# Kernel optimization log

Hardware: AMD Instinct MI355X
Metric: run time of the kernel (lower is better)

The kernel has to match this reference:

```python
import jax, jax.numpy as jnp
import numpy as np

NH, NW = 5, 5          # attn_neighborhood_size (odd -> symmetric 'same' padding)
HEADS, HEAD_DIM = 8, 64
DIM = 512              # == heads*head_dim, but project_out=True since heads>1
B, HMAP, WMAP = 4, 64, 64
N = HMAP * WMAP


def local_expand(t, height, width):
    """Equivalent of impulse-filter conv2d neighbor gather.

    t: [b, heads, n, d] -> [b, heads, n, NH*NW, d]
    neighbor f=(i,j) of pixel (p,q) is t[p+i-NH//2, q+j-NW//2], zero-padded.
    """
    b, h, n, d = t.shape
    y = t.reshape(b, h, height, width, d)
    ph, pw = NH // 2, NW // 2
    yp = jnp.pad(y, ((0, 0), (0, 0), (ph, ph), (pw, pw), (0, 0)))
    # fixed small loop over the 25 window offsets (row-major = filter order)
    slabs = [yp[:, :, i:i + height, j:j + width, :]
             for i in range(NH) for j in range(NW)]
    out = jnp.stack(slabs, axis=4)  # [b, h, H, W, F, d]
    return out.reshape(b, h, n, NH * NW, d)


def setup_inputs() -> dict:
    key = jax.random.key(0)
    k1, k2, k3, k4 = jax.random.split(key, 4)
    inner = HEADS * HEAD_DIM
    x = jax.random.normal(k1, (B, N, DIM), dtype=jnp.float32)
    # torch Linear weights are [out_features, in_features]
    w_qkv = jax.random.normal(k2, (3 * inner, DIM), dtype=jnp.float32) * (DIM ** -0.5)
    w_out = jax.random.normal(k3, (DIM, inner), dtype=jnp.float32) * (inner ** -0.5)
    b_out = jax.random.normal(k4, (DIM,), dtype=jnp.float32) * 0.01
    return {"x": x, "w_qkv": w_qkv, "w_out": w_out, "b_out": b_out,
            "h": HMAP, "w": WMAP}


def reference(x, w_qkv, w_out, b_out, h, w):
    b, n, _ = x.shape
    scale = HEAD_DIM ** -0.5
    qkv = x @ w_qkv.T                                   # [b, n, 3*inner]
    q, k, v = jnp.split(qkv, 3, axis=-1)
    def to_heads(t):
        return t.reshape(b, n, HEADS, HEAD_DIM).transpose(0, 2, 1, 3)  # b h n d
    q, k, v = to_heads(q), to_heads(k), to_heads(v)
    k_loc = local_expand(k, h, w)                       # [b, h, n, F, d]
    v_loc = local_expand(v, h, w)
    dots = jnp.einsum('bhnd,bhnfd->bhnf', q, k_loc) * scale
    attn = jax.nn.softmax(dots, axis=-1)
    out = jnp.einsum('bhnf,bhnfd->bhnd', attn, v_loc)   # [b, h, n, d]
    out = out.transpose(0, 2, 1, 3).reshape(b, n, HEADS * HEAD_DIM)
    return out @ w_out.T + b_out                        # dropout=0 (eval)
```

## Files before the change

### kernel.cpp

```cpp
#include <hip/hip_runtime.h>
#include <cstddef>
#include <cstdint>


namespace {

typedef short s16x8 __attribute__((ext_vector_type(8)));
typedef unsigned short u16x8 __attribute__((ext_vector_type(8)));
typedef float f32x4 __attribute__((ext_vector_type(4)));

constexpr int kHeads = 8;
constexpr int kN = 4096;
constexpr float kScale = 0.125f;

__device__ inline float b2f(unsigned short u) {
  return __uint_as_float((unsigned)u << 16);
}
__device__ inline float blo(unsigned u) {
  return __uint_as_float(u << 16);
}
__device__ inline float bhi(unsigned u) {
  return __uint_as_float(u & 0xffff0000u);
}
__device__ inline unsigned short f2b(float x) {
  unsigned u = __float_as_uint(x);
  return (unsigned short)((u + 0x7fffu + ((u >> 16) & 1u)) >> 16);
}

__device__ __forceinline__ float dot2bf(float d, unsigned a, unsigned b) {
  asm("v_dot2_f32_bf16 %0, %1, %2, %0" : "+v"(d) : "v"(a), "v"(b));
  return d;
}

__device__ __forceinline__ void g2l16(const unsigned short* g,
                                      unsigned short* l) {
  __builtin_amdgcn_global_load_lds(
      (const __attribute__((address_space(1))) void*)g,
      (__attribute__((address_space(3))) void*)l, 16, 0, 0);
}

__global__ __launch_bounds__(256) void cvt_all(
    const float* __restrict__ wq, const float* __restrict__ wo,
    const float* __restrict__ x, unsigned short* __restrict__ wqb,
    unsigned short* __restrict__ wob, unsigned short* __restrict__ xb) {
  const int i = blockIdx.x * 256 + threadIdx.x;
  const float* src;
  unsigned short* dst;
  int off;
  if (i < 98304) {
    src = wq; dst = wqb; off = i;
  } else if (i < 131072) {
    src = wo; dst = wob; off = i - 98304;
  } else {
    src = x; dst = xb; off = i - 131072;
  }
  const float4 a = ((const float4*)src)[off * 2];
  const float4 b = ((const float4*)src)[off * 2 + 1];
  u16x8 o;
  o[0] = f2b(a.x); o[1] = f2b(a.y); o[2] = f2b(a.z); o[3] = f2b(a.w);
  o[4] = f2b(b.x); o[5] = f2b(b.y); o[6] = f2b(b.z); o[7] = f2b(b.w);
  *(u16x8*)(dst + (size_t)off * 8) = o;
}

__device__ __forceinline__ void mfma_512(const unsigned short* __restrict__ A,
                                         const unsigned short* __restrict__ W,
                                         int m0, int n0, int tid,
                                         unsigned short* As, unsigned short* Bs,
                                         f32x4 (&acc)[4][4]) {
  const int lane = tid & 63;
  const int wv = tid >> 6;
  const int wm = wv & 1, wn = wv >> 1;
  const int rsub = lane >> 3;
  const int slog = (lane & 7) ^ rsub;
#pragma unroll
  for (int i = 0; i < 4; ++i)
#pragma unroll
    for (int j = 0; j < 4; ++j) acc[i][j] = f32x4{0.f, 0.f, 0.f, 0.f};

  for (int k0 = 0; k0 < 512; k0 += 64) {
#pragma unroll
    for (int it = 0; it < 4; ++it) {
      const int g = wv * 4 + it;
      const int row = g * 8 + rsub;
      g2l16(A + (size_t)(m0 + row) * 512 + k0 + slog * 8, As + g * 512);
      g2l16(W + (size_t)(n0 + row) * 512 + k0 + slog * 8, Bs + g * 512);
    }
    __syncthreads();
#pragma unroll
    for (int kh = 0; kh < 2; ++kh) {
      s16x8 af[4], bf[4];
      const int q = kh * 4 + (lane >> 4);
#pragma unroll
      for (int i = 0; i < 4; ++i) {
        const int Ra = wm * 64 + i * 16 + (lane & 15);
        af[i] = *(const s16x8*)&As[Ra * 64 + ((q ^ (Ra & 7)) * 8)];
        const int Rb = wn * 64 + i * 16 + (lane & 15);
        bf[i] = *(const s16x8*)&Bs[Rb * 64 + ((q ^ (Rb & 7)) * 8)];
      }
#pragma unroll
      for (int i = 0; i < 4; ++i)
#pragma unroll
        for (int j = 0; j < 4; ++j)
          acc[i][j] = __builtin_amdgcn_mfma_f32_16x16x32_bf16(
              af[i], bf[j], acc[i][j], 0, 0, 0);
    }
    __syncthreads();
  }
}

__global__ __launch_bounds__(256, 3) void gemm_qkv(
    const unsigned short* __restrict__ A, const unsigned short* __restrict__ W,
    unsigned short* __restrict__ Qb, unsigned short* __restrict__ Kb,
    unsigned short* __restrict__ Vb) {
  __shared__ unsigned short As[8192], Bs[8192];
  const int tid = threadIdx.x;
  const int id = blockIdx.x;
  const int xcd = id & 7;
  const int j = id >> 3;
  const int by = xcd * 16 + j / 12;
  const int bx = j % 12;
  f32x4 acc[4][4];
  mfma_512(A, W, by * 128, bx * 128, tid, As, Bs, acc);

  const int lane = tid & 63;
  const int wv = tid >> 6;
  const int wm = wv & 1, wn = wv >> 1;
  const int cn = bx * 128 + wn * 64;
  unsigned short* dst = (cn < 512) ? Qb : (cn < 1024 ? Kb : Vb);
  const int head = (cn >> 6) & 7;
  const int colb = lane & 15;
#pragma unroll
  for (int mi = 0; mi < 4; ++mi) {
#pragma unroll
    for (int r = 0; r < 4; ++r) {
      const int m = by * 128 + wm * 64 + mi * 16 + (lane >> 4) * 4 + r;
      const int b = m >> 12;
      const int p = m & 4095;
      unsigned short* o =
          dst + ((size_t)(b * kHeads + head) * kN + p) * 64 + colb;
#pragma unroll
      for (int ni = 0; ni < 4; ++ni) o[ni * 16] = f2b(acc[mi][ni][r]);
    }
  }
}

__global__ __launch_bounds__(256, 3) void gemm_out(
    const unsigned short* __restrict__ A, const unsigned short* __restrict__ W,
    const float* __restrict__ bias, float* __restrict__ out) {
  __shared__ unsigned short As[8192], Bs[8192];
  const int tid = threadIdx.x;
  const int id = blockIdx.x;
  const int xcd = id & 7;
  const int j = id >> 3;
  const int by = xcd * 16 + (j >> 2);
  const int bx = j & 3;
  f32x4 acc[4][4];
  mfma_512(A, W, by * 128, bx * 128, tid, As, Bs, acc);

  const int lane = tid & 63;
  const int wv = tid >> 6;
  const int wm = wv & 1, wn = wv >> 1;
  float bvr[4];
#pragma unroll
  for (int ni = 0; ni < 4; ++ni)
    bvr[ni] = bias[bx * 128 + wn * 64 + ni * 16 + (lane & 15)];
#pragma unroll
  for (int mi = 0; mi < 4; ++mi) {
#pragma unroll
    for (int r = 0; r < 4; ++r) {
      const int m = by * 128 + wm * 64 + mi * 16 + (lane >> 4) * 4 + r;
      float* o = out + (size_t)m * 512 + bx * 128 + wn * 64 + (lane & 15);
#pragma unroll
      for (int ni = 0; ni < 4; ++ni) o[ni * 16] = acc[mi][ni][r] + bvr[ni];
    }
  }
}

__global__ __launch_bounds__(256) void attn_q4(
    const unsigned short* __restrict__ Q, const unsigned short* __restrict__ K,
    const unsigned short* __restrict__ V, unsigned short* __restrict__ AO) {
  __shared__ unsigned short H[144 * 64];
  const int tid = threadIdx.x;
  const int id = blockIdx.x;
  const int xcd = id & 7;
  const int k8 = id >> 3;
  const int bh = xcd * 4 + (k8 >> 6);
  const int tile = k8 & 63;
  const int ty0 = (tile >> 3) * 8, tx0 = (tile & 7) * 8;
  const size_t base = (size_t)bh * kN;
  const int pix = tid >> 2;
  const int sub = tid & 3;
  const int pyl = pix >> 3, pxl = pix & 7;
  const int p = (ty0 + pyl) * 64 + tx0 + pxl;

  const unsigned short* qp = Q + (base + p) * 64 + sub * 16;
  const uint4 qa = *(const uint4*)qp;
  const uint4 qb = *(const uint4*)(qp + 8);

  for (int i = tid; i < 1152; i += 256) {
    const int r = i >> 3, c = i & 7;
    const int gy = ty0 - 2 + r / 12;
    const int gx = tx0 - 2 + r % 12;
    u16x8 v = {};
    if ((unsigned)gy < 64u && (unsigned)gx < 64u)
      v = *(const u16x8*)(K + (base + gy * 64 + gx) * 64 + c * 8);
    *(u16x8*)&H[r * 64 + ((c * 8) ^ ((r & 7) << 3))] = v;
  }
  __syncthreads();

  float dots[25];
#pragma unroll
  for (int fy = 0; fy < 5; ++fy) {
#pragma unroll
    for (int fx = 0; fx < 5; ++fx) {
      const int row = (pyl + fy) * 12 + pxl + fx;
      const int swz = (row & 7) << 3;
      const unsigned short* hr = &H[row * 64];
      const uint4 ka = *(const uint4*)(hr + ((sub * 16) ^ swz));
      const uint4 kb = *(const uint4*)(hr + ((sub * 16 + 8) ^ swz));
      float d = 0.f;
      d = dot2bf(d, qa.x, ka.x);
      d = dot2bf(d, qa.y, ka.y);
      d = dot2bf(d, qa.z, ka.z);
      d = dot2bf(d, qa.w, ka.w);
      d = dot2bf(d, qb.x, kb.x);
      d = dot2bf(d, qb.y, kb.y);
      d = dot2bf(d, qb.z, kb.z);
      d = dot2bf(d, qb.w, kb.w);
      dots[fy * 5 + fx] = d;
    }
  }

#pragma unroll
  for (int f = 0; f < 25; ++f) {
    dots[f] += __shfl_xor(dots[f], 1, 64);
    dots[f] += __shfl_xor(dots[f], 2, 64);
  }

  float mx = -1e30f;
#pragma unroll
  for (int f = 0; f < 25; ++f) {
    dots[f] *= kScale;
    mx = fmaxf(mx, dots[f]);
  }
  float sum = 0.f;
#pragma unroll
  for (int f = 0; f < 25; ++f) {
    dots[f] = __expf(dots[f] - mx);
    sum += dots[f];
  }
  const float inv = 1.f / sum;
#pragma unroll
  for (int f = 0; f < 25; ++f) dots[f] *= inv;

  __syncthreads();
  for (int i = tid; i < 1152; i += 256) {
    const int r = i >> 3, c = i & 7;
    const int gy = ty0 - 2 + r / 12;
    const int gx = tx0 - 2 + r % 12;
    u16x8 v = {};
    if ((unsigned)gy < 64u && (unsigned)gx < 64u)
      v = *(const u16x8*)(V + (base + gy * 64 + gx) * 64 + c * 8);
    *(u16x8*)&H[r * 64 + ((c * 8) ^ ((r & 7) << 3))] = v;
  }
  __syncthreads();

  const int b = bh >> 3, h = bh & 7;
  unsigned short* op = AO + ((size_t)(b * kN + p)) * 512 + h * 64 + sub * 16;
#pragma unroll 1
  for (int hh = 0; hh < 2; ++hh) {
    float o[8];
#pragma unroll
    for (int j = 0; j < 8; ++j) o[j] = 0.f;
#pragma unroll
    for (int fy = 0; fy < 5; ++fy) {
#pragma unroll
      for (int fx = 0; fx < 5; ++fx) {
        const int row = (pyl + fy) * 12 + pxl + fx;
        const int swz = (row & 7) << 3;
        const uint4 va =
            *(const uint4*)&H[row * 64 + ((sub * 16 + hh * 8) ^ swz)];
        const float wf = dots[fy * 5 + fx];
        o[0] = fmaf(wf, blo(va.x), o[0]);
        o[1] = fmaf(wf, bhi(va.x), o[1]);
        o[2] = fmaf(wf, blo(va.y), o[2]);
        o[3] = fmaf(wf, bhi(va.y), o[3]);
        o[4] = fmaf(wf, blo(va.z), o[4]);
        o[5] = fmaf(wf, bhi(va.z), o[5]);
        o[6] = fmaf(wf, blo(va.w), o[6]);
        o[7] = fmaf(wf, bhi(va.w), o[7]);
      }
    }
    u16x8 pk;
#pragma unroll
    for (int j = 0; j < 8; ++j) pk[j] = f2b(o[j]);
    *(u16x8*)(op + hh * 8) = pk;
  }
}

}

extern "C" void kernel_launch(void* const* d_in, const int* in_sizes, int n_in,
                              void* d_out, int out_size, void* d_ws,
                              size_t ws_size, hipStream_t stream) {
  (void)in_sizes; (void)n_in; (void)out_size; (void)ws_size;
  const float* x = (const float*)d_in[0];
  const float* w_qkv = (const float*)d_in[1];
  const float* w_out = (const float*)d_in[2];
  const float* b_out = (const float*)d_in[3];
  float* out = (float*)d_out;

  unsigned short* ws0 = (unsigned short*)d_ws;
  unsigned short* wqkvb = ws0;
  unsigned short* woutb = ws0 + 786432;
  unsigned short* xb = ws0 + 1048576;
  unsigned short* Qb = ws0 + 9437184;
  unsigned short* Kb = ws0 + 17825792;
  unsigned short* Vb = ws0 + 26214400;
  unsigned short* AO = ws0 + 34603008;

  cvt_all<<<4608, 256, 0, stream>>>(w_qkv, w_out, x, wqkvb, woutb, xb);
  gemm_qkv<<<1536, 256, 0, stream>>>(xb, wqkvb, Qb, Kb, Vb);
  attn_q4<<<2048, 256, 0, stream>>>(Qb, Kb, Vb, AO);
  gemm_out<<<512, 256, 0, stream>>>(AO, woutb, b_out, out);
}
```

Baseline: 173.4 us.

## Prefetch K and V halos together via async global-to-LDS loads

The attention kernel now issues both the K and V halo tiles at the start as direct global-to-LDS loads into a double-sized shared buffer. It waits only on the K loads before computing the dot products and softmax, so the V loads overlap that compute. Out-of-bounds neighbours read from a small zero buffer that cvt_all clears, since the async LDS load cannot write zeros itself. This doubles LDS use per block, which may lower occupancy, and relies on per-wave lane-ordered LDS placement and a hand-counted vmcnt.

```diff
diff --git a/kernel.cpp b/kernel.cpp
--- a/kernel.cpp
+++ b/kernel.cpp
@@ -13,9 +13,6 @@
 constexpr int kN = 4096;
 constexpr float kScale = 0.125f;
 
-__device__ inline float b2f(unsigned short u) {
-  return __uint_as_float((unsigned)u << 16);
-}
 __device__ inline float blo(unsigned u) {
   return __uint_as_float(u << 16);
 }
@@ -42,8 +39,10 @@
 __global__ __launch_bounds__(256) void cvt_all(
     const float* __restrict__ wq, const float* __restrict__ wo,
     const float* __restrict__ x, unsigned short* __restrict__ wqb,
-    unsigned short* __restrict__ wob, unsigned short* __restrict__ xb) {
+    unsigned short* __restrict__ wob, unsigned short* __restrict__ xb,
+    unsigned short* __restrict__ zp) {
   const int i = blockIdx.x * 256 + threadIdx.x;
+  if (i < 16) ((unsigned long long*)zp)[i] = 0ull;
   const float* src;
   unsigned short* dst;
   int off;
@@ -178,10 +177,12 @@
 
 __global__ __launch_bounds__(256) void attn_q4(
     const unsigned short* __restrict__ Q, const unsigned short* __restrict__ K,
-    const unsigned short* __restrict__ V, unsigned short* __restrict__ AO) {
-  __shared__ unsigned short H[144 * 64];
+    const unsigned short* __restrict__ V, const unsigned short* __restrict__ Zp,
+    unsigned short* __restrict__ AO) {
+  __shared__ unsigned short H[2 * 144 * 64];
   const int tid = threadIdx.x;
   const int id = blockIdx.x;
+  const int wv = tid >> 6;
   const int xcd = id & 7;
   const int k8 = id >> 3;
   const int bh = xcd * 4 + (k8 >> 6);
@@ -197,16 +198,40 @@
   const uint4 qa = *(const uint4*)qp;
   const uint4 qb = *(const uint4*)(qp + 8);
 
-  for (int i = tid; i < 1152; i += 256) {
-    const int r = i >> 3, c = i & 7;
-    const int gy = ty0 - 2 + r / 12;
-    const int gx = tx0 - 2 + r % 12;
-    u16x8 v = {};
-    if ((unsigned)gy < 64u && (unsigned)gx < 64u)
-      v = *(const u16x8*)(K + (base + gy * 64 + gx) * 64 + c * 8);
-    *(u16x8*)&H[r * 64 + ((c * 8) ^ ((r & 7) << 3))] = v;
-  }
-  __syncthreads();
+#pragma unroll
+  for (int it = 0; it < 5; ++it) {
+    const int i = it * 256 + tid;
+    if (i < 1152) {
+      const int r = i >> 3;
+      const int cg = (tid & 7) ^ (r & 7);
+      const int gy = ty0 - 2 + r / 12;
+      const int gx = tx0 - 2 + r % 12;
+      const unsigned short* src =
+          ((unsigned)gy < 64u && (unsigned)gx < 64u)
+              ? K + (base + (size_t)(gy * 64 + gx)) * 64 + cg * 8
+              : Zp + cg * 8;
+      g2l16(src, &H[(it * 32 + wv * 8) * 64]);
+    }
+  }
+#pragma unroll
+  for (int it = 0; it < 5; ++it) {
+    const int i = it * 256 + tid;
+    if (i < 1152) {
+      const int r = i >> 3;
+      const int cg = (tid & 7) ^ (r & 7);
+      const int gy = ty0 - 2 + r / 12;
+      const int gx = tx0 - 2 + r % 12;
+      const unsigned short* src =
+          ((unsigned)gy < 64u && (unsigned)gx < 64u)
+              ? V + (base + (size_t)(gy * 64 + gx)) * 64 + cg * 8
+              : Zp + cg * 8;
+      g2l16(src, &H[9216 + (it * 32 + wv * 8) * 64]);
+    }
+  }
+
+  asm volatile("s_waitcnt vmcnt(4)" ::: "memory");
+  __builtin_amdgcn_s_barrier();
+  __builtin_amdgcn_sched_barrier(0);
 
   float dots[25];
 #pragma unroll
@@ -253,17 +278,9 @@
 #pragma unroll
   for (int f = 0; f < 25; ++f) dots[f] *= inv;
 
-  __syncthreads();
-  for (int i = tid; i < 1152; i += 256) {
-    const int r = i >> 3, c = i & 7;
-    const int gy = ty0 - 2 + r / 12;
-    const int gx = tx0 - 2 + r % 12;
-    u16x8 v = {};
-    if ((unsigned)gy < 64u && (unsigned)gx < 64u)
-      v = *(const u16x8*)(V + (base + gy * 64 + gx) * 64 + c * 8);
-    *(u16x8*)&H[r * 64 + ((c * 8) ^ ((r & 7) << 3))] = v;
-  }
-  __syncthreads();
+  asm volatile("s_waitcnt vmcnt(0)" ::: "memory");
+  __builtin_amdgcn_s_barrier();
+  __builtin_amdgcn_sched_barrier(0);
 
   const int b = bh >> 3, h = bh & 7;
   unsigned short* op = AO + ((size_t)(b * kN + p)) * 512 + h * 64 + sub * 16;
@@ -279,7 +296,7 @@
         const int row = (pyl + fy) * 12 + pxl + fx;
         const int swz = (row & 7) << 3;
         const uint4 va =
-            *(const uint4*)&H[row * 64 + ((sub * 16 + hh * 8) ^ swz)];
+            *(const uint4*)&H[9216 + row * 64 + ((sub * 16 + hh * 8) ^ swz)];
         const float wf = dots[fy * 5 + fx];
         o[0] = fmaf(wf, blo(va.x), o[0]);
         o[1] = fmaf(wf, bhi(va.x), o[1]);
@@ -318,9 +335,10 @@
   unsigned short* Kb = ws0 + 17825792;
   unsigned short* Vb = ws0 + 26214400;
   unsigned short* AO = ws0 + 34603008;
-
-  cvt_all<<<4608, 256, 0, stream>>>(w_qkv, w_out, x, wqkvb, woutb, xb);
+  unsigned short* Zp = ws0 + 42991616;
+
+  cvt_all<<<4608, 256, 0, stream>>>(w_qkv, w_out, x, wqkvb, woutb, xb, Zp);
   gemm_qkv<<<1536, 256, 0, stream>>>(xb, wqkvb, Qb, Kb, Vb);
-  attn_q4<<<2048, 256, 0, stream>>>(Qb, Kb, Vb, AO);
+  attn_q4<<<2048, 256, 0, stream>>>(Qb, Kb, Vb, Zp, AO);
   gemm_out<<<512, 256, 0, stream>>>(AO, woutb, b_out, out);
 }
```

Measured after the change: 164.7 us, median of 2. 1.05x faster.
